# Kernel optimization log

Measured on AMD Instinct MI355X. Metric: run time of the kernel, lower is better.

Reference implementation:

```python
import jax, jax.numpy as jnp
import numpy as np

B, S, H = 16, 4096, 768
NUM_WORDS = S // 2  # 2048: max distinct words per sample (padded output width)


def setup_inputs() -> dict:
    key = jax.random.key(0)
    k1, k2 = jax.random.split(key)
    hidden_states = jax.random.normal(k1, (B, S, H), dtype=jnp.float32)
    # word ids: non-decreasing, contiguous from 0; -1 marks special tokens (None in HF)
    inc = jax.random.bernoulli(k2, 0.5, (B, S)).astype(jnp.int32)
    inc = inc.at[:, :2].set(0)  # keep word 0 alive at position 1 after masking CLS
    word_ids = jnp.maximum(jnp.cumsum(inc, axis=1) - 1, 0)
    word_ids = jnp.minimum(word_ids, NUM_WORDS - 1)  # static cap on segment count
    word_ids = word_ids.at[:, 0].set(-1)   # [CLS]
    word_ids = word_ids.at[:, -1].set(-1)  # [SEP]
    return {"hidden_states": hidden_states, "word_ids": word_ids}


def reference(hidden_states, word_ids):
    # Segment-mean of subword embeddings into word embeddings.
    # hidden_states: [B, S, H] float; word_ids: [B, S] int, -1 = special token (dropped).
    b, s, h = hidden_states.shape
    valid = word_ids >= 0  # [B, S]
    # offset per-sample word ids into a flat segment space of size B*NUM_WORDS;
    # invalid tokens go to segment (b*NUM_WORDS + 0) but contribute zeros.
    wid = jnp.where(valid, word_ids, 0)
    seg = (wid + jnp.arange(b, dtype=word_ids.dtype)[:, None] * NUM_WORDS).reshape(-1)
    data = jnp.where(valid[..., None], hidden_states, 0.0).reshape(b * s, h)
    sums = jax.ops.segment_sum(data, seg, num_segments=b * NUM_WORDS)
    counts = jax.ops.segment_sum(
        valid.reshape(-1).astype(hidden_states.dtype), seg, num_segments=b * NUM_WORDS
    )
    sums = sums.reshape(b, NUM_WORDS, h)
    counts = counts.reshape(b, NUM_WORDS)
    # mean per word; words with zero tokens stay 0 (matches pad_sequence zero-padding)
    return sums / jnp.maximum(counts, 1.0)[..., None]
```

## Files before the change

### kernel.cpp

```cpp
#include <hip/hip_runtime.h>

constexpr int B = 16;
constexpr int S = 4096;
constexpr int H = 768;
constexpr int NW = 2048;
constexpr int V4 = H / 4;
constexpr int W = 8;
constexpr int WPS = 512;
constexpr int WAVES_PER_BLK = 4;

__device__ __forceinline__ void acc4(float4& a, const float4 v) {
    a.x += v.x; a.y += v.y; a.z += v.z; a.w += v.w;
}

__global__ __launch_bounds__(256)
void seg_mean_kernel(const float* __restrict__ hs,
                     const int* __restrict__ wid,
                     float* __restrict__ out) {
    const int wave = threadIdx.x >> 6;
    const int lane = threadIdx.x & 63;
    const int gwin = blockIdx.x * WAVES_PER_BLK + wave;
    const int b = gwin >> 9;
    const int win = gwin & (WPS - 1);
    const int t0 = 1 + win * W;

    const int* __restrict__ wrow = wid + (size_t)b * S;

    int gidx = t0 - 1 + lane;
    if (gidx > S - 1) gidx = S - 1;
    if (lane == 63) gidx = S - 2;
    const int wv = wrow[gidx];

    const float4* __restrict__ base = (const float4*)(hs + (size_t)b * S * H);
#define TOKS(X) X(0) X(1) X(2) X(3) X(4) X(5) X(6) X(7)
#define DECL(J) float4 rA##J, rB##J, rC##J;
    TOKS(DECL)
#define LOADTOK(J) { int t = t0 + J; if (t > S - 2) t = S - 2;              \
        const float4* p = base + (size_t)t * V4;                           \
        rA##J = p[lane]; rB##J = p[lane + 64]; rC##J = p[lane + 128]; }
    TOKS(LOADTOK)
    __builtin_amdgcn_sched_barrier(0);

    const int maxw = __builtin_amdgcn_readlane(wv, 63);

    const int wprev = __shfl_up(wv, 1);
    const bool chg = (lane >= 1) && (lane <= 62) && (wv != wprev);
    const unsigned long long mask = __ballot(chg);

    const float4 z = make_float4(0.f, 0.f, 0.f, 0.f);
    float4 a0 = z, a1 = z, a2 = z;
    int cnt = 0, wcur = 0;
    bool active = false;

    auto flush = [&]() {
        const float inv = 1.0f / (float)cnt;
        float4 m0 = a0, m1 = a1, m2 = a2;
        m0.x *= inv; m0.y *= inv; m0.z *= inv; m0.w *= inv;
        m1.x *= inv; m1.y *= inv; m1.z *= inv; m1.w *= inv;
        m2.x *= inv; m2.y *= inv; m2.z *= inv; m2.w *= inv;
        float4* o = (float4*)(out + ((size_t)b * NW + wcur) * H);
        o[lane] = m0; o[lane + 64] = m1; o[lane + 128] = m2;
    };

#define STEP(J) {                                                          \
        if ((mask >> (J + 1)) & 1ull) {                                    \
            if (active) flush();                                           \
            const int wval = __builtin_amdgcn_readlane(wv, J + 1);         \
            active = (wval >= 0);                                          \
            if (active) { wcur = wval; a0 = z; a1 = z; a2 = z; cnt = 0; }  \
        }                                                                  \
        if (active) { acc4(a0, rA##J); acc4(a1, rB##J); acc4(a2, rC##J); ++cnt; } }
    TOKS(STEP)
#undef STEP
#undef LOADTOK
#undef DECL
#undef TOKS

    if (active) {
        int end;
        const unsigned long long hi = mask >> 9;
        if (hi) {
            end = t0 + 8 + __builtin_ctzll(hi);
        } else {
            end = t0 + 62;
            while (true) {
                int t = end + lane;
                if (t > S - 1) t = S - 1;
                const int wv2 = wrow[t];
                const unsigned long long m2 = __ballot(wv2 != wcur);
                if (m2) { end += __builtin_ctzll(m2); break; }
                end += 64;
            }
        }
        cnt += end - (t0 + 8);
        int t = t0 + 8;
        for (; t + 3 < end; t += 4) {
            const float4* p0 = base + (size_t)t * V4;
            const float4* p1 = p0 + V4;
            const float4* p2 = p1 + V4;
            const float4* p3 = p2 + V4;
            float4 x00 = p0[lane], x01 = p0[lane + 64], x02 = p0[lane + 128];
            float4 x10 = p1[lane], x11 = p1[lane + 64], x12 = p1[lane + 128];
            float4 x20 = p2[lane], x21 = p2[lane + 64], x22 = p2[lane + 128];
            float4 x30 = p3[lane], x31 = p3[lane + 64], x32 = p3[lane + 128];
            acc4(a0, x00); acc4(a1, x01); acc4(a2, x02);
            acc4(a0, x10); acc4(a1, x11); acc4(a2, x12);
            acc4(a0, x20); acc4(a1, x21); acc4(a2, x22);
            acc4(a0, x30); acc4(a1, x31); acc4(a2, x32);
        }
        for (; t < end; ++t) {
            const float4* p = base + (size_t)t * V4;
            float4 v0 = p[lane], v1 = p[lane + 64], v2 = p[lane + 128];
            acc4(a0, v0); acc4(a1, v1); acc4(a2, v2);
        }
        flush();
    }

    {
        const int wz0 = win * 4;
#pragma unroll
        for (int k = 0; k < 4; ++k) {
            const int w = wz0 + k;
            if (w > maxw) {
                float4* o = (float4*)(out + ((size_t)b * NW + w) * H);
                o[lane] = z; o[lane + 64] = z; o[lane + 128] = z;
            }
        }
    }
}

extern "C" void kernel_launch(void* const* d_in, const int* in_sizes, int n_in,
                              void* d_out, int out_size, void* d_ws, size_t ws_size,
                              hipStream_t stream) {
    const float* hs = (const float*)d_in[0];
    const int* wid = (const int*)d_in[1];
    float* out = (float*)d_out;

    seg_mean_kernel<<<(B * WPS) / WAVES_PER_BLK, 64 * WAVES_PER_BLK, 0, stream>>>(
        hs, wid, out);
}
```

Measured before the change: 309.8 us.

## Process 32-token chunks per wave with double-buffered register prefetch

Each wave now handles 32 tokens instead of 8. It keeps two register banks of 8 tokens each, loading the next bank while consuming the current one. The aim is to amortise per-wave setup, keep more loads in flight to hide memory latency, and cut the number of waves. In exchange it uses many more VGPRs, which lowers occupancy, and leaves far fewer waves in the grid.

```diff
diff --git a/kernel.cpp b/kernel.cpp
--- a/kernel.cpp
+++ b/kernel.cpp
@@ -5,8 +5,8 @@
 constexpr int H = 768;
 constexpr int NW = 2048;
 constexpr int V4 = H / 4;
-constexpr int W = 8;
-constexpr int WPS = 512;
+constexpr int T = 32;
+constexpr int CPS = 128;
 constexpr int WAVES_PER_BLK = 4;
 
 __device__ __forceinline__ void acc4(float4& a, const float4 v) {
@@ -19,10 +19,10 @@
                      float* __restrict__ out) {
     const int wave = threadIdx.x >> 6;
     const int lane = threadIdx.x & 63;
-    const int gwin = blockIdx.x * WAVES_PER_BLK + wave;
-    const int b = gwin >> 9;
-    const int win = gwin & (WPS - 1);
-    const int t0 = 1 + win * W;
+    const int gc = blockIdx.x * WAVES_PER_BLK + wave;
+    const int b = gc >> 7;
+    const int chunk = gc & (CPS - 1);
+    const int t0 = 1 + chunk * T;
 
     const int* __restrict__ wrow = wid + (size_t)b * S;
 
@@ -32,13 +32,21 @@
     const int wv = wrow[gidx];
 
     const float4* __restrict__ base = (const float4*)(hs + (size_t)b * S * H);
-#define TOKS(X) X(0) X(1) X(2) X(3) X(4) X(5) X(6) X(7)
-#define DECL(J) float4 rA##J, rB##J, rC##J;
-    TOKS(DECL)
-#define LOADTOK(J) { int t = t0 + J; if (t > S - 2) t = S - 2;              \
+
+#define SLOTS(X) X(0) X(1) X(2) X(3) X(4) X(5) X(6) X(7)
+#define DECLP(J) float4 pA##J, pB##J, pC##J;
+#define DECLQ(J) float4 qA##J, qB##J, qC##J;
+    SLOTS(DECLP)
+    SLOTS(DECLQ)
+
+#define LOAD1(R, J, TB) { int t = (TB) + J; if (t > S - 2) t = S - 2;      \
         const float4* p = base + (size_t)t * V4;                           \
-        rA##J = p[lane]; rB##J = p[lane + 64]; rC##J = p[lane + 128]; }
-    TOKS(LOADTOK)
+        R##A##J = p[lane]; R##B##J = p[lane + 64]; R##C##J = p[lane + 128]; }
+#define ISSUE(R, TB) LOAD1(R,0,TB) LOAD1(R,1,TB) LOAD1(R,2,TB) LOAD1(R,3,TB) \
+                     LOAD1(R,4,TB) LOAD1(R,5,TB) LOAD1(R,6,TB) LOAD1(R,7,TB)
+
+    ISSUE(p, t0)
+    ISSUE(q, t0 + 8)
     __builtin_amdgcn_sched_barrier(0);
 
     const int maxw = __builtin_amdgcn_readlane(wv, 63);
@@ -62,25 +70,41 @@
         o[lane] = m0; o[lane + 64] = m1; o[lane + 128] = m2;
     };
 
-#define STEP(J) {                                                          \
-        if ((mask >> (J + 1)) & 1ull) {                                    \
+#define STEPX(BIT, RA, RB, RC) {                                           \
+        if ((mask >> (BIT)) & 1ull) {                                      \
             if (active) flush();                                           \
-            const int wval = __builtin_amdgcn_readlane(wv, J + 1);         \
+            const int wval = __builtin_amdgcn_readlane(wv, (BIT));         \
             active = (wval >= 0);                                          \
             if (active) { wcur = wval; a0 = z; a1 = z; a2 = z; cnt = 0; }  \
         }                                                                  \
-        if (active) { acc4(a0, rA##J); acc4(a1, rB##J); acc4(a2, rC##J); ++cnt; } }
-    TOKS(STEP)
-#undef STEP
-#undef LOADTOK
-#undef DECL
-#undef TOKS
+        if (active) { acc4(a0, RA); acc4(a1, RB); acc4(a2, RC); ++cnt; } }
+#define CONSUME(BB, R) \
+    STEPX((BB)+1, R##A0, R##B0, R##C0) STEPX((BB)+2, R##A1, R##B1, R##C1)  \
+    STEPX((BB)+3, R##A2, R##B2, R##C2) STEPX((BB)+4, R##A3, R##B3, R##C3)  \
+    STEPX((BB)+5, R##A4, R##B4, R##C4) STEPX((BB)+6, R##A5, R##B5, R##C5)  \
+    STEPX((BB)+7, R##A6, R##B6, R##C6) STEPX((BB)+8, R##A7, R##B7, R##C7)
+
+    CONSUME(0, p)
+    ISSUE(p, t0 + 16)
+    __builtin_amdgcn_sched_barrier(0);
+    CONSUME(8, q)
+    ISSUE(q, t0 + 24)
+    __builtin_amdgcn_sched_barrier(0);
+    CONSUME(16, p)
+    CONSUME(24, q)
+#undef CONSUME
+#undef STEPX
+#undef ISSUE
+#undef LOAD1
+#undef DECLP
+#undef DECLQ
+#undef SLOTS
 
     if (active) {
         int end;
-        const unsigned long long hi = mask >> 9;
+        const unsigned long long hi = mask >> 33;
         if (hi) {
-            end = t0 + 8 + __builtin_ctzll(hi);
+            end = t0 + 32 + __builtin_ctzll(hi);
         } else {
             end = t0 + 62;
             while (true) {
@@ -92,8 +116,8 @@
                 end += 64;
             }
         }
-        cnt += end - (t0 + 8);
-        int t = t0 + 8;
+        cnt += end - (t0 + 32);
+        int t = t0 + 32;
         for (; t + 3 < end; t += 4) {
             const float4* p0 = base + (size_t)t * V4;
             const float4* p1 = p0 + V4;
@@ -117,9 +141,9 @@
     }
 
     {
-        const int wz0 = win * 4;
+        const int wz0 = chunk * 16;
 #pragma unroll
-        for (int k = 0; k < 4; ++k) {
+        for (int k = 0; k < 16; ++k) {
             const int w = wz0 + k;
             if (w > maxw) {
                 float4* o = (float4*)(out + ((size_t)b * NW + w) * H);
@@ -136,6 +160,6 @@
     const int* wid = (const int*)d_in[1];
     float* out = (float*)d_out;
 
-    seg_mean_kernel<<<(B * WPS) / WAVES_PER_BLK, 64 * WAVES_PER_BLK, 0, stream>>>(
+    seg_mean_kernel<<<(B * CPS) / WAVES_PER_BLK, 64 * WAVES_PER_BLK, 0, stream>>>(
         hs, wid, out);
 }
```

Result: no change. 312.2 us (+0.8%).
